# Performance work log

Hardware: AMD Instinct MI355X
Metric: run time of the kernel (lower is better)

Reference implementation:

```python
import jax, jax.numpy as jnp
from jax import lax
import numpy as np


def _conv3x3(x, w, b):
    # x: [B,C,H,W], w: [O,I,3,3] (OIHW), SAME padding, stride 1
    y = lax.conv_general_dilated(x, w, window_strides=(1, 1), padding='SAME',
                                 dimension_numbers=('NCHW', 'OIHW', 'NCHW'))
    return y + b[None, :, None, None]


def setup_inputs() -> dict:
    key = jax.random.key(0)
    ks = jax.random.split(key, 9)
    B, C, H, W = 4, 64, 64, 64
    wscale = 1.0 / np.sqrt(C * 9)  # keep conv outputs / attention logits sane
    x = jax.random.normal(ks[0], (B, C, H, W), dtype=jnp.float32)
    wq = jax.random.normal(ks[1], (C, C, 3, 3), dtype=jnp.float32) * wscale
    bq = jax.random.normal(ks[2], (C,), dtype=jnp.float32) * 0.1
    wk = jax.random.normal(ks[3], (C, C, 3, 3), dtype=jnp.float32) * wscale
    bk = jax.random.normal(ks[4], (C,), dtype=jnp.float32) * 0.1
    wv = jax.random.normal(ks[5], (C, C, 3, 3), dtype=jnp.float32) * wscale
    bv = jax.random.normal(ks[6], (C,), dtype=jnp.float32) * 0.1
    pos_gamma = jax.random.normal(ks[7], (1,), dtype=jnp.float32)
    chan_gamma = jax.random.normal(ks[8], (1,), dtype=jnp.float32)
    return {'x': x, 'wq': wq, 'bq': bq, 'wk': wk, 'bk': bk, 'wv': wv, 'bv': bv,
            'pos_gamma': pos_gamma, 'chan_gamma': chan_gamma}


def reference(x, wq, bq, wk, bk, wv, bv, pos_gamma, chan_gamma):
    B, C, H, W = x.shape
    N = H * W
    # position (spatial) self-attention over N = H*W locations
    q = _conv3x3(x, wq, bq).reshape(B, C, N)
    k = _conv3x3(x, wk, bk).reshape(B, C, N)
    v = _conv3x3(x, wv, bv).reshape(B, C, N)
    # attn[b,i,j] = softmax_j( sum_c q[b,c,i] * k[b,c,j] )
    pos_attn = jax.nn.softmax(jnp.einsum('bci,bcj->bij', q, k), axis=-1)
    # pos_out[b,c,j] = sum_i v[b,c,i] * attn[b,i,j]  (matches torch.bmm(v, attn))
    pos = jnp.einsum('bci,bij->bcj', v, pos_attn).reshape(B, C, H, W)
    pos_out = pos_gamma * pos + x
    # channel self-attention over C channels (x is its own q/k/v)
    xf = x.reshape(B, C, N)
    chan_attn = jax.nn.softmax(jnp.einsum('bcn,bdn->bcd', xf, xf), axis=-1)
    chan = jnp.einsum('bcd,bdn->bcn', chan_attn, xf).reshape(B, C, H, W)
    chan_out = chan_gamma * chan + x
    return pos_out + chan_out
```

## Files before the change

kernel.cpp:

```cpp
#include <hip/hip_runtime.h>

#define OFF_LP    0u
#define OFF_OP1   0u
#define OFF_XV2   65536u
#define OFF_GP    589824u
#define OFF_Q2    1048576u
#define OFF_K2    2097152u
#define OFF_V2    3145728u
#define OFF_X2    3670016u
#define OFF_WT    4194304u
#define OFF_A     4730880u
#define WS_FLOATS 4747264u

typedef short s8v __attribute__((ext_vector_type(8)));
typedef float f16v __attribute__((ext_vector_type(16)));

#define MFMA32(a, b, c) __builtin_amdgcn_mfma_f32_32x32x16_bf16((a), (b), (c), 0, 0, 0)

__device__ __forceinline__ unsigned short bf16_rne(float f) {
    union { float f; unsigned int u; } v; v.f = f;
    unsigned int r = v.u + 0x7FFFu + ((v.u >> 16) & 1u);
    return (unsigned short)(r >> 16);
}
__device__ __forceinline__ float bf2f(unsigned short h) {
    union { unsigned int u; float f; } t; t.u = ((unsigned int)h) << 16;
    return t.f;
}
__device__ __forceinline__ void split2(float f, unsigned short& h, unsigned short& l) {
    unsigned short hh = bf16_rne(f);
    h = hh;
    l = bf16_rne(f - bf2f(hh));
}
__device__ __forceinline__ unsigned int cvtpk(float lo, float hi) {
    unsigned int r;
    asm("v_cvt_pk_bf16_f32 %0, %1, %2" : "=v"(r) : "v"(lo), "v"(hi));
    return r;
}
__device__ __forceinline__ void pl32swap(unsigned int& a, unsigned int& b) {
    asm volatile("v_permlane32_swap_b32 %0, %1" : "+v"(a), "+v"(b));
}
__device__ __forceinline__ s8v mk8(unsigned int w0, unsigned int w1,
                                   unsigned int w2, unsigned int w3) {
    union { unsigned int u[4]; s8v v; } t;
    t.u[0] = w0; t.u[1] = w1; t.u[2] = w2; t.u[3] = w3;
    return t.v;
}
__device__ __forceinline__ f16v zero16() {
    f16v z;
#pragma unroll
    for (int i = 0; i < 16; ++i) z[i] = 0.0f;
    return z;
}


__global__ __launch_bounds__(256) void k_prep(
        const float* __restrict__ wq, const float* __restrict__ wk,
        const float* __restrict__ wv, const float* __restrict__ x,
        unsigned short* __restrict__ wf, unsigned short* __restrict__ X2,
        unsigned short* __restrict__ XV2) {
    int bid = blockIdx.x, tid = threadIdx.x;
    if (bid < 432) {
        int t = bid * 256 + tid;
        int f = t >> 9, pos = t & 511;
        int lane = pos >> 3, e = pos & 7;
        int oc = f & 1, kst = (f >> 1) & 3;
        int ct = f >> 3;
        int tap = ct % 9, conv = ct / 9;
        int o = oc * 32 + (lane & 31);
        int ci = kst * 16 + (lane >> 5) * 8 + e;
        const float* w = (conv == 0) ? wq : (conv == 1) ? wk : wv;
        float v = w[(o * 64 + ci) * 9 + tap];
        unsigned short hh, ll;
        split2(v, hh, ll);
        wf[(f * 2 + 0) * 512 + pos] = hh;
        wf[(f * 2 + 1) * 512 + pos] = ll;
    } else {
        int gid = (bid - 432) * 256 + tid;
        int b = gid >> 16;
        int c = (gid >> 10) & 63;
        int n4 = (gid & 1023) * 4;
        float4 v = *(const float4*)(x + (size_t)(b * 64 + c) * 4096 + n4);
        unsigned short hv[4] = {bf16_rne(v.x), bf16_rne(v.y), bf16_rne(v.z), bf16_rne(v.w)};
        int kst = c >> 4, e = c & 7, hb = (c >> 3) & 1;
#pragma unroll
        for (int u = 0; u < 4; ++u) {
            int n = n4 + u;
            int nch = n >> 5, lane = (n & 31) + 32 * hb;
            X2[(size_t)((b * 128 + nch) * 4 + kst) * 512 + lane * 8 + e] = hv[u];
        }
        int ich = n4 >> 5, ksub = (n4 >> 4) & 1, cb = c >> 5;
        int lane2 = (c & 31) + 32 * ((n4 >> 3) & 1);
        size_t xi = (size_t)(((b * 128 + ich) * 2 + ksub) * 2 + cb) * 512 + lane2 * 8 + (n4 & 7);
        unsigned long long w = (unsigned long long)hv[0]
                             | ((unsigned long long)hv[1] << 16)
                             | ((unsigned long long)hv[2] << 32)
                             | ((unsigned long long)hv[3] << 48);
        *(unsigned long long*)(XV2 + xi) = w;
    }
}

__global__ __launch_bounds__(384) void k_conv(
        const float* __restrict__ x, const unsigned short* __restrict__ wf,
        const float* __restrict__ bq, const float* __restrict__ bk, const float* __restrict__ bv,
        unsigned short* __restrict__ Q2, unsigned short* __restrict__ K2,
        unsigned short* __restrict__ V2) {
    int nb = blockIdx.x;
    int b = blockIdx.y;
    int h = nb >> 1, w0 = (nb & 1) * 32;

    __shared__ unsigned short xwh[6528];
    __shared__ unsigned short xwl[6528];

    int tid = threadIdx.x;
    for (int idx = tid; idx < 6528; idx += 384) {
        int W = idx % 34;
        int c = (idx / 34) & 63;
        int dy = idx / (34 * 64);
        int hs = h + dy - 1, wi = w0 + W - 1;
        float v = 0.0f;
        if (hs >= 0 && hs < 64 && wi >= 0 && wi < 64)
            v = x[((b * 64 + c) * 64 + hs) * 64 + wi];
        unsigned short hh_, ll_;
        split2(v, hh_, ll_);
        int row = dy * 34 + W;
        int byt = row * 128 + c * 2;
        int swz = byt ^ ((row & 7) << 4);
        *(unsigned short*)((char*)xwh + swz) = hh_;
        *(unsigned short*)((char*)xwl + swz) = ll_;
    }
    __syncthreads();

    int lane = tid & 63, wv = tid >> 6;
    int conv = wv >> 1, oc = wv & 1;
    int hh = lane >> 5, l31 = lane & 31;

    const float* bias = (conv == 0) ? bq : (conv == 1) ? bk : bv;
    f16v D;
    if (conv < 2) {
#pragma unroll
        for (int r = 0; r < 16; ++r)
            D[r] = bias[oc * 32 + (r & 3) + 8 * (r >> 2) + 4 * hh];
    } else {
        float bvv = bias[oc * 32 + l31];
#pragma unroll
        for (int r = 0; r < 16; ++r) D[r] = bvv;
    }

#pragma unroll
    for (int tap = 0; tap < 9; ++tap) {
        int dy = tap / 3, dx = tap % 3;
#pragma unroll
        for (int kst = 0; kst < 4; ++kst) {
            int f = ((conv * 9 + tap) * 4 + kst) * 2 + oc;
            s8v Wh = *(const s8v*)(wf + (f * 2 + 0) * 512 + lane * 8);
            s8v Wl = *(const s8v*)(wf + (f * 2 + 1) * 512 + lane * 8);
            int row = dy * 34 + dx + l31;
            int byt = row * 128 + kst * 32 + hh * 16;
            int swz = byt ^ ((row & 7) << 4);
            s8v Xh = *(const s8v*)((const char*)xwh + swz);
            s8v Xl = *(const s8v*)((const char*)xwl + swz);
            if (conv < 2) {
                D = MFMA32(Wh, Xh, D);
                D = MFMA32(Wh, Xl, D);
                D = MFMA32(Wl, Xh, D);
            } else {
                D = MFMA32(Xh, Wh, D);
                D = MFMA32(Xl, Wh, D);
                D = MFMA32(Xh, Wl, D);
            }
        }
    }

    if (conv < 2) {
        unsigned short sh[16], sl[16];
#pragma unroll
        for (int r = 0; r < 16; ++r) split2(D[r], sh[r], sl[r]);
        unsigned int ah0 = sh[0] | ((unsigned int)sh[1] << 16), ah1 = sh[2] | ((unsigned int)sh[3] << 16);
        unsigned int ah2 = sh[4] | ((unsigned int)sh[5] << 16), ah3 = sh[6] | ((unsigned int)sh[7] << 16);
        pl32swap(ah0, ah2); pl32swap(ah1, ah3);
        s8v F0h = mk8(ah0, ah1, ah2, ah3);
        unsigned int al0 = sl[0] | ((unsigned int)sl[1] << 16), al1 = sl[2] | ((unsigned int)sl[3] << 16);
        unsigned int al2 = sl[4] | ((unsigned int)sl[5] << 16), al3 = sl[6] | ((unsigned int)sl[7] << 16);
        pl32swap(al0, al2); pl32swap(al1, al3);
        s8v F0l = mk8(al0, al1, al2, al3);
        unsigned int bh0 = sh[8] | ((unsigned int)sh[9] << 16), bh1 = sh[10] | ((unsigned int)sh[11] << 16);
        unsigned int bh2 = sh[12] | ((unsigned int)sh[13] << 16), bh3 = sh[14] | ((unsigned int)sh[15] << 16);
        pl32swap(bh0, bh2); pl32swap(bh1, bh3);
        s8v F1h = mk8(bh0, bh1, bh2, bh3);
        unsigned int bl0 = sl[8] | ((unsigned int)sl[9] << 16), bl1 = sl[10] | ((unsigned int)sl[11] << 16);
        unsigned int bl2 = sl[12] | ((unsigned int)sl[13] << 16), bl3 = sl[14] | ((unsigned int)sl[15] << 16);
        pl32swap(bl0, bl2); pl32swap(bl1, bl3);
        s8v F1l = mk8(bl0, bl1, bl2, bl3);
        unsigned short* dst = (conv == 0) ? Q2 : K2;
        size_t b0 = (size_t)(((b * 128 + nb) * 4 + oc * 2 + 0) * 2) * 512 + lane * 8;
        size_t b1 = (size_t)(((b * 128 + nb) * 4 + oc * 2 + 1) * 2) * 512 + lane * 8;
        *(s8v*)(dst + b0) = F0h;
        *(s8v*)(dst + b0 + 512) = F0l;
        *(s8v*)(dst + b1) = F1h;
        *(s8v*)(dst + b1 + 512) = F1l;
    } else {
        unsigned int a0 = cvtpk(D[0], D[1]),  a1 = cvtpk(D[2], D[3]);
        unsigned int a2 = cvtpk(D[4], D[5]),  a3 = cvtpk(D[6], D[7]);
        pl32swap(a0, a2); pl32swap(a1, a3);
        s8v F0h = mk8(a0, a1, a2, a3);
        unsigned int b0w = cvtpk(D[8], D[9]),  b1w = cvtpk(D[10], D[11]);
        unsigned int b2w = cvtpk(D[12], D[13]), b3w = cvtpk(D[14], D[15]);
        pl32swap(b0w, b2w); pl32swap(b1w, b3w);
        s8v F1h = mk8(b0w, b1w, b2w, b3w);
        size_t v0 = (size_t)(((b * 128 + nb) * 2 + 0) * 2 + oc) * 512 + lane * 8;
        size_t v1 = (size_t)(((b * 128 + nb) * 2 + 1) * 2 + oc) * 512 + lane * 8;
        *(s8v*)(V2 + v0) = F0h;
        *(s8v*)(V2 + v1) = F1h;
    }
}

__global__ __launch_bounds__(256) void k_gram(const unsigned short* __restrict__ XV2,
                                              float* __restrict__ Gp) {
    int kp = blockIdx.x, b = blockIdx.y;
    int tid = threadIdx.x, lane = tid & 63, wv = tid >> 6;
    int cb1 = wv & 1, cb2 = wv >> 1;
    f16v G = zero16();
#pragma unroll
    for (int t = 0; t < 8; ++t) {
        int ich = kp * 8 + t;
        const unsigned short* base = XV2 + (size_t)(b * 128 + ich) * 2048 + lane * 8;
        s8v a0 = *(const s8v*)(base + (0 * 2 + cb1) * 512);
        s8v b0 = *(const s8v*)(base + (0 * 2 + cb2) * 512);
        s8v a1 = *(const s8v*)(base + (1 * 2 + cb1) * 512);
        s8v b1 = *(const s8v*)(base + (1 * 2 + cb2) * 512);
        G = MFMA32(a0, b0, G);
        G = MFMA32(a1, b1, G);
    }
    int hh = lane >> 5, l31 = lane & 31;
#pragma unroll
    for (int r = 0; r < 16; ++r) {
        int cc = cb1 * 32 + (r & 3) + 8 * (r >> 2) + 4 * hh;
        int dd = cb2 * 32 + l31;
        Gp[(size_t)(kp * 4 + b) * 4096 + cc * 64 + dd] = G[r];
    }
}

__global__ void k_asm(const float* __restrict__ Gp, unsigned short* __restrict__ A2) {
    int row = blockIdx.x;
    int d = threadIdx.x;
    int b = row >> 6, c = row & 63;
    float g = 0.0f;
#pragma unroll
    for (int p = 0; p < 16; ++p) g += Gp[(size_t)(p * 4 + b) * 4096 + c * 64 + d];
    float mx = g;
    for (int off = 32; off >= 1; off >>= 1) mx = fmaxf(mx, __shfl_xor(mx, off, 64));
    float e = __expf(g - mx);
    float s = e;
    for (int off = 32; off >= 1; off >>= 1) s += __shfl_xor(s, off, 64);
    float a = e / s;
    int cb = c >> 5, kst = d >> 4;
    int lane2 = (c & 31) + 32 * ((d >> 3) & 1);
    A2[(size_t)((b * 2 + cb) * 4 + kst) * 512 + lane2 * 8 + (d & 7)] = bf16_rne(a);
}

__global__ __launch_bounds__(512, 2) void k_pass1(
        const unsigned short* __restrict__ Q2, const unsigned short* __restrict__ K2,
        float* __restrict__ lpart) {
    int flat = blockIdx.x;
    int xcd = flat & 7;
    int b = xcd >> 1;
    int rest = (xcd & 1) * 64 + (flat >> 3);
    int ichp = rest & 63, jh = rest >> 6;
    int ich0 = ichp * 2;
    int tid = threadIdx.x, lane = tid & 63, wv = tid >> 6;

    __shared__ float lsum[8][2][32];

    const unsigned short* qp = Q2 + (size_t)(b * 128 + ich0) * 4096 + lane * 8;
    s8v q0f0 = *(const s8v*)(qp);
    s8v q0f1 = *(const s8v*)(qp + 512);
    s8v q0f2 = *(const s8v*)(qp + 1024);
    s8v q0f3 = *(const s8v*)(qp + 1536);
    s8v q0f4 = *(const s8v*)(qp + 2048);
    s8v q0f5 = *(const s8v*)(qp + 2560);
    s8v q0f6 = *(const s8v*)(qp + 3072);
    s8v q0f7 = *(const s8v*)(qp + 3584);
    s8v q1f0 = *(const s8v*)(qp + 4096);
    s8v q1f1 = *(const s8v*)(qp + 4608);
    s8v q1f2 = *(const s8v*)(qp + 5120);
    s8v q1f3 = *(const s8v*)(qp + 5632);
    s8v q1f4 = *(const s8v*)(qp + 6144);
    s8v q1f5 = *(const s8v*)(qp + 6656);
    s8v q1f6 = *(const s8v*)(qp + 7168);
    s8v q1f7 = *(const s8v*)(qp + 7680);

    float la0 = 0.f, la1 = 0.f, lb0 = 0.f, lb1 = 0.f;
#pragma unroll 1
    for (int t = 0; t < 8; ++t) {
        int jch = jh * 64 + wv * 8 + t;
        const unsigned short* kp = K2 + (size_t)(b * 128 + jch) * 4096 + lane * 8;
        s8v kf0 = *(const s8v*)(kp);
        s8v kf1 = *(const s8v*)(kp + 512);
        s8v kf2 = *(const s8v*)(kp + 1024);
        s8v kf3 = *(const s8v*)(kp + 1536);
        s8v kf4 = *(const s8v*)(kp + 2048);
        s8v kf5 = *(const s8v*)(kp + 2560);
        s8v kf6 = *(const s8v*)(kp + 3072);
        s8v kf7 = *(const s8v*)(kp + 3584);
        {
            f16v Sa = zero16(), Sb = zero16();
            Sa = MFMA32(kf0, q0f0, Sa);
            Sa = MFMA32(kf0, q0f1, Sa);
            Sa = MFMA32(kf1, q0f0, Sa);
            Sa = MFMA32(kf2, q0f2, Sa);
            Sa = MFMA32(kf2, q0f3, Sa);
            Sa = MFMA32(kf3, q0f2, Sa);
            Sb = MFMA32(kf4, q0f4, Sb);
            Sb = MFMA32(kf4, q0f5, Sb);
            Sb = MFMA32(kf5, q0f4, Sb);
            Sb = MFMA32(kf6, q0f6, Sb);
            Sb = MFMA32(kf6, q0f7, Sb);
            Sb = MFMA32(kf7, q0f6, Sb);
#pragma unroll
            for (int r = 0; r < 8; ++r) la0 += __expf(Sa[r] + Sb[r]);
#pragma unroll
            for (int r = 8; r < 16; ++r) la1 += __expf(Sa[r] + Sb[r]);
        }
        {
            f16v Sa = zero16(), Sb = zero16();
            Sa = MFMA32(kf0, q1f0, Sa);
            Sa = MFMA32(kf0, q1f1, Sa);
            Sa = MFMA32(kf1, q1f0, Sa);
            Sa = MFMA32(kf2, q1f2, Sa);
            Sa = MFMA32(kf2, q1f3, Sa);
            Sa = MFMA32(kf3, q1f2, Sa);
            Sb = MFMA32(kf4, q1f4, Sb);
            Sb = MFMA32(kf4, q1f5, Sb);
            Sb = MFMA32(kf5, q1f4, Sb);
            Sb = MFMA32(kf6, q1f6, Sb);
            Sb = MFMA32(kf6, q1f7, Sb);
            Sb = MFMA32(kf7, q1f6, Sb);
#pragma unroll
            for (int r = 0; r < 8; ++r) lb0 += __expf(Sa[r] + Sb[r]);
#pragma unroll
            for (int r = 8; r < 16; ++r) lb1 += __expf(Sa[r] + Sb[r]);
        }
    }
    float lacc0 = la0 + la1;
    lacc0 += __shfl_xor(lacc0, 32);
    float lacc1 = lb0 + lb1;
    lacc1 += __shfl_xor(lacc1, 32);
    if (lane < 32) {
        lsum[wv][0][lane] = lacc0;
        lsum[wv][1][lane] = lacc1;
    }
    __syncthreads();
    if (tid < 64) {
        int ic = tid >> 5, iL = tid & 31;
        float s = 0.f;
#pragma unroll
        for (int p = 0; p < 8; ++p) s += lsum[p][ic][iL];
        lpart[jh * 16384 + b * 4096 + (ich0 + ic) * 32 + iL] = s;
    }
}

__global__ __launch_bounds__(256) void k_mvn(
        unsigned short* __restrict__ V2, const float* __restrict__ lpart) {
    int u = blockIdx.x * 256 + threadIdx.x;
    int lane = u & 63, ksub = (u >> 7) & 1;
    int ich = (u >> 8) & 127, b = u >> 15;
    int n0 = ich * 32 + ksub * 16 + (lane >> 5) * 8;
    size_t base = (size_t)u * 8;
    s8v vh = *(s8v*)(V2 + base);
    const float* l0 = lpart + b * 4096 + n0;
    float4 a0 = *(const float4*)(l0);
    float4 a1 = *(const float4*)(l0 + 4);
    float4 c0 = *(const float4*)(l0 + 16384);
    float4 c1 = *(const float4*)(l0 + 16384 + 4);
    float lv[8] = {a0.x + c0.x, a0.y + c0.y, a0.z + c0.z, a0.w + c0.w,
                   a1.x + c1.x, a1.y + c1.y, a1.z + c1.z, a1.w + c1.w};
    s8v o;
#pragma unroll
    for (int e = 0; e < 8; ++e) {
        float inv = 1.0f / lv[e];
        o[e] = (short)bf16_rne(bf2f((unsigned short)vh[e]) * inv);
    }
    *(s8v*)(V2 + base) = o;
}

__global__ __launch_bounds__(512, 2) void k_pass2(
        const unsigned short* __restrict__ Q2, const unsigned short* __restrict__ K2,
        const unsigned short* __restrict__ V2, float* __restrict__ outp,
        float* __restrict__ op1) {
    int flat = blockIdx.x;
    int xcd = flat & 7;
    int b = xcd >> 1;
    int rest = (xcd & 1) * 64 + (flat >> 3);
    int jtp = rest & 63, ih = rest >> 6;
    int jt0 = jtp * 2;
    int tid = threadIdx.x, lane = tid & 63, wv = tid >> 6;

    __shared__ float smem[12288];
    unsigned short* Klds = (unsigned short*)(smem + 8192);
    float* rl = smem;

    {
        const unsigned short* ksrc = K2 + (size_t)(b * 128 + jt0) * 4096;
#pragma unroll
        for (int s = 0; s < 2; ++s) {
            int seg = tid + s * 512;
            *(s8v*)(Klds + seg * 8) = *(const s8v*)(ksrc + seg * 8);
        }
    }
    __syncthreads();

    f16v O0a = zero16(), O1a = zero16();
    f16v O0b = zero16(), O1b = zero16();

#pragma unroll 1
    for (int t = 0; t < 8; ++t) {
        int ich = ih * 64 + wv * 8 + t;
        const unsigned short* qp = Q2 + (size_t)(b * 128 + ich) * 4096 + lane * 8;
        s8v qf0 = *(const s8v*)(qp);
        s8v qf1 = *(const s8v*)(qp + 512);
        s8v qf2 = *(const s8v*)(qp + 1024);
        s8v qf3 = *(const s8v*)(qp + 1536);
        s8v qf4 = *(const s8v*)(qp + 2048);
        s8v qf5 = *(const s8v*)(qp + 2560);
        s8v qf6 = *(const s8v*)(qp + 3072);
        s8v qf7 = *(const s8v*)(qp + 3584);
        const unsigned short* vp = V2 + (size_t)(b * 128 + ich) * 2048 + lane * 8;
        s8v vA = *(const s8v*)(vp);
        s8v vB = *(const s8v*)(vp + 512);
        s8v vC = *(const s8v*)(vp + 1024);
        s8v vD = *(const s8v*)(vp + 1536);

#pragma unroll
        for (int js = 0; js < 2; ++js) {
            const unsigned short* kl = Klds + js * 4096 + lane * 8;
            s8v kf0 = *(const s8v*)(kl);
            s8v kf1 = *(const s8v*)(kl + 512);
            s8v kf2 = *(const s8v*)(kl + 1024);
            s8v kf3 = *(const s8v*)(kl + 1536);
            s8v kf4 = *(const s8v*)(kl + 2048);
            s8v kf5 = *(const s8v*)(kl + 2560);
            s8v kf6 = *(const s8v*)(kl + 3072);
            s8v kf7 = *(const s8v*)(kl + 3584);

            f16v Sa = zero16(), Sb = zero16();
            Sa = MFMA32(qf0, kf0, Sa);
            Sa = MFMA32(qf0, kf1, Sa);
            Sa = MFMA32(qf1, kf0, Sa);
            Sa = MFMA32(qf2, kf2, Sa);
            Sa = MFMA32(qf2, kf3, Sa);
            Sa = MFMA32(qf3, kf2, Sa);
            Sb = MFMA32(qf4, kf4, Sb);
            Sb = MFMA32(qf4, kf5, Sb);
            Sb = MFMA32(qf5, kf4, Sb);
            Sb = MFMA32(qf6, kf6, Sb);
            Sb = MFMA32(qf6, kf7, Sb);
            Sb = MFMA32(qf7, kf6, Sb);

            float p[16];
#pragma unroll
            for (int r = 0; r < 16; ++r) p[r] = __expf(Sa[r] + Sb[r]);

            unsigned int a0 = cvtpk(p[0], p[1]),  a1 = cvtpk(p[2], p[3]);
            unsigned int a2 = cvtpk(p[4], p[5]),  a3 = cvtpk(p[6], p[7]);
            pl32swap(a0, a2);
            pl32swap(a1, a3);
            s8v P0 = mk8(a0, a1, a2, a3);
            unsigned int b0 = cvtpk(p[8], p[9]),  b1 = cvtpk(p[10], p[11]);
            unsigned int b2 = cvtpk(p[12], p[13]), b3 = cvtpk(p[14], p[15]);
            pl32swap(b0, b2);
            pl32swap(b1, b3);
            s8v P1 = mk8(b0, b1, b2, b3);

            if (js == 0) {
                O0a = MFMA32(vA, P0, O0a);
                O0a = MFMA32(vC, P1, O0a);
                O1a = MFMA32(vB, P0, O1a);
                O1a = MFMA32(vD, P1, O1a);
            } else {
                O0b = MFMA32(vA, P0, O0b);
                O0b = MFMA32(vC, P1, O0b);
                O1b = MFMA32(vB, P0, O1b);
                O1b = MFMA32(vD, P1, O1b);
            }
        }
    }

    int hh = lane >> 5, jj = lane & 31;
    float s0[4], s1[4];
    if (wv < 4) {
#pragma unroll
        for (int r = 0; r < 16; ++r) {
            int c = (r & 3) + 8 * (r >> 2) + 4 * hh;
            rl[(wv * 64 + c) * 32 + jj] = O0a[r];
            rl[(wv * 64 + c + 32) * 32 + jj] = O1a[r];
        }
    }
    __syncthreads();
#pragma unroll
    for (int k = 0; k < 4; ++k) {
        int el = tid + k * 512;
        s0[k] = ((rl[el] + rl[2048 + el]) + rl[4096 + el]) + rl[6144 + el];
    }
    __syncthreads();
    if (wv >= 4) {
#pragma unroll
        for (int r = 0; r < 16; ++r) {
            int c = (r & 3) + 8 * (r >> 2) + 4 * hh;
            rl[((wv - 4) * 64 + c) * 32 + jj] = O0a[r];
            rl[((wv - 4) * 64 + c + 32) * 32 + jj] = O1a[r];
        }
    }
    __syncthreads();
#pragma unroll
    for (int k = 0; k < 4; ++k) {
        int el = tid + k * 512;
        s0[k] = ((s0[k] + rl[el]) + rl[2048 + el]) + rl[4096 + el];
        s0[k] += rl[6144 + el];
    }
    __syncthreads();
    if (wv < 4) {
#pragma unroll
        for (int r = 0; r < 16; ++r) {
            int c = (r & 3) + 8 * (r >> 2) + 4 * hh;
            rl[(wv * 64 + c) * 32 + jj] = O0b[r];
            rl[(wv * 64 + c + 32) * 32 + jj] = O1b[r];
        }
    }
    __syncthreads();
#pragma unroll
    for (int k = 0; k < 4; ++k) {
        int el = tid + k * 512;
        s1[k] = ((rl[el] + rl[2048 + el]) + rl[4096 + el]) + rl[6144 + el];
    }
    __syncthreads();
    if (wv >= 4) {
#pragma unroll
        for (int r = 0; r < 16; ++r) {
            int c = (r & 3) + 8 * (r >> 2) + 4 * hh;
            rl[((wv - 4) * 64 + c) * 32 + jj] = O0b[r];
            rl[((wv - 4) * 64 + c + 32) * 32 + jj] = O1b[r];
        }
    }
    __syncthreads();
#pragma unroll
    for (int k = 0; k < 4; ++k) {
        int el = tid + k * 512;
        s1[k] = ((s1[k] + rl[el]) + rl[2048 + el]) + rl[4096 + el];
        s1[k] += rl[6144 + el];
    }

    float* dst = ih ? op1 : outp;
#pragma unroll
    for (int k = 0; k < 4; ++k) {
        int el = tid + k * 512;
        int c = el >> 5, j2 = el & 31;
        size_t ob = (size_t)(b * 64 + c) * 4096 + jtp * 64;
        dst[ob + j2] = s0[k];
        dst[ob + 32 + j2] = s1[k];
    }
}

__global__ __launch_bounds__(256) void k_final(
        const float* __restrict__ op1, const unsigned short* __restrict__ X2,
        const unsigned short* __restrict__ A2, const float* __restrict__ x,
        const float* __restrict__ pg, const float* __restrict__ cg,
        float* __restrict__ out) {
    int flat = blockIdx.x;
    int xcd = flat & 7;
    int b = xcd >> 1;
    int jtp = (xcd & 1) * 32 + (flat >> 3);
    int jt0 = jtp * 2;
    int tid = threadIdx.x, lane = tid & 63, wv = tid >> 6;
    int hh = lane >> 5, jj = lane & 31;

    __shared__ float chan[64 * 65];

    {
        int jts = wv >> 1, cb = wv & 1;
        f16v Dc = zero16();
#pragma unroll
        for (int kst = 0; kst < 4; ++kst) {
            s8v af = *(const s8v*)(A2 + (size_t)((b * 2 + cb) * 4 + kst) * 512 + lane * 8);
            s8v xf = *(const s8v*)(X2 + (size_t)((b * 128 + jt0 + jts) * 4 + kst) * 512 + lane * 8);
            Dc = MFMA32(af, xf, Dc);
        }
#pragma unroll
        for (int r = 0; r < 16; ++r) {
            int c = cb * 32 + (r & 3) + 8 * (r >> 2) + 4 * hh;
            chan[c * 65 + jts * 32 + jj] = Dc[r];
        }
    }
    __syncthreads();
    float pgv = pg[0], cgv = cg[0];
#pragma unroll
    for (int k = 0; k < 16; ++k) {
        int el = tid + k * 256;
        int c = el >> 6, j2 = el & 63;
        size_t loc = (size_t)(b * 64 + c) * 4096 + jtp * 64 + j2;
        float pos = out[loc] + op1[loc];
        out[loc] = pgv * pos + cgv * chan[c * 65 + j2] + 2.0f * x[loc];
    }
}

extern "C" void kernel_launch(void* const* d_in, const int* in_sizes, int n_in,
                              void* d_out, int out_size, void* d_ws, size_t ws_size,
                              hipStream_t stream) {
    const float* x  = (const float*)d_in[0];
    const float* wq = (const float*)d_in[1];
    const float* bq = (const float*)d_in[2];
    const float* wk = (const float*)d_in[3];
    const float* bk = (const float*)d_in[4];
    const float* wv = (const float*)d_in[5];
    const float* bv = (const float*)d_in[6];
    const float* pg = (const float*)d_in[7];
    const float* cg = (const float*)d_in[8];
    float* out = (float*)d_out;

    if (ws_size < (size_t)WS_FLOATS * sizeof(float)) return;
    float* ws = (float*)d_ws;
    float* lpart = ws + OFF_LP;
    float* op1   = ws + OFF_OP1;
    unsigned short* XV2 = (unsigned short*)(ws + OFF_XV2);
    float* Gp = ws + OFF_GP;
    unsigned short* Q2  = (unsigned short*)(ws + OFF_Q2);
    unsigned short* K2  = (unsigned short*)(ws + OFF_K2);
    unsigned short* V2  = (unsigned short*)(ws + OFF_V2);
    unsigned short* X2  = (unsigned short*)(ws + OFF_X2);
    unsigned short* wfb = (unsigned short*)(ws + OFF_WT);
    unsigned short* A2  = (unsigned short*)(ws + OFF_A);

    k_prep<<<1456, 256, 0, stream>>>(wq, wk, wv, x, wfb, X2, XV2);
    k_conv<<<dim3(128, 4), 384, 0, stream>>>(x, wfb, bq, bk, bv, Q2, K2, V2);
    k_gram<<<dim3(16, 4), 256, 0, stream>>>(XV2, Gp);
    k_asm<<<256, 64, 0, stream>>>(Gp, A2);
    k_pass1<<<512, 512, 0, stream>>>(Q2, K2, lpart);
    k_mvn<<<512, 256, 0, stream>>>(V2, lpart);
    k_pass2<<<512, 512, 0, stream>>>(Q2, K2, V2, out, op1);
    k_final<<<256, 256, 0, stream>>>(op1, X2, A2, x, pg, cg, out);
}
```

Measured before the change: 115.8 us.

## Fuse final epilogue into pass2 and drop the split over query halves

```diff
diff --git a/kernel.cpp b/kernel.cpp
--- a/kernel.cpp
+++ b/kernel.cpp
@@ -1,7 +1,6 @@
 #include <hip/hip_runtime.h>
 
 #define OFF_LP    0u
-#define OFF_OP1   0u
 #define OFF_XV2   65536u
 #define OFF_GP    589824u
 #define OFF_Q2    1048576u
@@ -383,15 +382,16 @@
     *(s8v*)(V2 + base) = o;
 }
 
-__global__ __launch_bounds__(512, 2) void k_pass2(
+__global__ __launch_bounds__(512) void k_pass2(
         const unsigned short* __restrict__ Q2, const unsigned short* __restrict__ K2,
-        const unsigned short* __restrict__ V2, float* __restrict__ outp,
-        float* __restrict__ op1) {
+        const unsigned short* __restrict__ V2, const unsigned short* __restrict__ X2,
+        const unsigned short* __restrict__ A2, const float* __restrict__ x,
+        const float* __restrict__ pg, const float* __restrict__ cg,
+        float* __restrict__ out) {
     int flat = blockIdx.x;
     int xcd = flat & 7;
     int b = xcd >> 1;
-    int rest = (xcd & 1) * 64 + (flat >> 3);
-    int jtp = rest & 63, ih = rest >> 6;
+    int jtp = (xcd & 1) * 32 + (flat >> 3);
     int jt0 = jtp * 2;
     int tid = threadIdx.x, lane = tid & 63, wv = tid >> 6;
 
@@ -412,9 +412,9 @@
     f16v O0a = zero16(), O1a = zero16();
     f16v O0b = zero16(), O1b = zero16();
 
-#pragma unroll 1
-    for (int t = 0; t < 8; ++t) {
-        int ich = ih * 64 + wv * 8 + t;
+#pragma unroll 2
+    for (int t = 0; t < 16; ++t) {
+        int ich = wv * 16 + t;
         const unsigned short* qp = Q2 + (size_t)(b * 128 + ich) * 4096 + lane * 8;
         s8v qf0 = *(const s8v*)(qp);
         s8v qf1 = *(const s8v*)(qp + 512);
@@ -548,57 +548,40 @@
         s1[k] = ((s1[k] + rl[el]) + rl[2048 + el]) + rl[4096 + el];
         s1[k] += rl[6144 + el];
     }
-
-    float* dst = ih ? op1 : outp;
+    __syncthreads();
+
+    float* chan = smem;
+    float* xres = smem + 4160;
+    if (wv < 4) {
+        int jts = wv >> 1, cb = wv & 1;
+        f16v Dc = zero16();
+#pragma unroll
+        for (int kst = 0; kst < 4; ++kst) {
+            s8v af = *(const s8v*)(A2 + (size_t)((b * 2 + cb) * 4 + kst) * 512 + lane * 8);
+            s8v xf = *(const s8v*)(X2 + (size_t)((b * 128 + jt0 + jts) * 4 + kst) * 512 + lane * 8);
+            Dc = MFMA32(af, xf, Dc);
+        }
+#pragma unroll
+        for (int r = 0; r < 16; ++r) {
+            int c = cb * 32 + (r & 3) + 8 * (r >> 2) + 4 * hh;
+            chan[c * 65 + jts * 32 + jj] = Dc[r];
+        }
+    }
+#pragma unroll
+    for (int k = 0; k < 8; ++k) {
+        int el = tid + k * 512;
+        int c = el >> 6, j2 = el & 63;
+        xres[el] = x[(size_t)(b * 64 + c) * 4096 + jtp * 64 + j2];
+    }
+    __syncthreads();
+    float pgv = pg[0], cgv = cg[0];
 #pragma unroll
     for (int k = 0; k < 4; ++k) {
         int el = tid + k * 512;
         int c = el >> 5, j2 = el & 31;
         size_t ob = (size_t)(b * 64 + c) * 4096 + jtp * 64;
-        dst[ob + j2] = s0[k];
-        dst[ob + 32 + j2] = s1[k];
-    }
-}
-
-__global__ __launch_bounds__(256) void k_final(
-        const float* __restrict__ op1, const unsigned short* __restrict__ X2,
-        const unsigned short* __restrict__ A2, const float* __restrict__ x,
-        const float* __restrict__ pg, const float* __restrict__ cg,
-        float* __restrict__ out) {
-    int flat = blockIdx.x;
-    int xcd = flat & 7;
-    int b = xcd >> 1;
-    int jtp = (xcd & 1) * 32 + (flat >> 3);
-    int jt0 = jtp * 2;
-    int tid = threadIdx.x, lane = tid & 63, wv = tid >> 6;
-    int hh = lane >> 5, jj = lane & 31;
-
-    __shared__ float chan[64 * 65];
-
-    {
-        int jts = wv >> 1, cb = wv & 1;
-        f16v Dc = zero16();
-#pragma unroll
-        for (int kst = 0; kst < 4; ++kst) {
-            s8v af = *(const s8v*)(A2 + (size_t)((b * 2 + cb) * 4 + kst) * 512 + lane * 8);
-            s8v xf = *(const s8v*)(X2 + (size_t)((b * 128 + jt0 + jts) * 4 + kst) * 512 + lane * 8);
-            Dc = MFMA32(af, xf, Dc);
-        }
-#pragma unroll
-        for (int r = 0; r < 16; ++r) {
-            int c = cb * 32 + (r & 3) + 8 * (r >> 2) + 4 * hh;
-            chan[c * 65 + jts * 32 + jj] = Dc[r];
-        }
-    }
-    __syncthreads();
-    float pgv = pg[0], cgv = cg[0];
-#pragma unroll
-    for (int k = 0; k < 16; ++k) {
-        int el = tid + k * 256;
-        int c = el >> 6, j2 = el & 63;
-        size_t loc = (size_t)(b * 64 + c) * 4096 + jtp * 64 + j2;
-        float pos = out[loc] + op1[loc];
-        out[loc] = pgv * pos + cgv * chan[c * 65 + j2] + 2.0f * x[loc];
+        out[ob + j2] = pgv * s0[k] + cgv * chan[c * 65 + j2] + 2.0f * xres[c * 64 + j2];
+        out[ob + 32 + j2] = pgv * s1[k] + cgv * chan[c * 65 + 32 + j2] + 2.0f * xres[c * 64 + 32 + j2];
     }
 }
 
@@ -619,7 +602,6 @@
     if (ws_size < (size_t)WS_FLOATS * sizeof(float)) return;
     float* ws = (float*)d_ws;
     float* lpart = ws + OFF_LP;
-    float* op1   = ws + OFF_OP1;
     unsigned short* XV2 = (unsigned short*)(ws + OFF_XV2);
     float* Gp = ws + OFF_GP;
     unsigned short* Q2  = (unsigned short*)(ws + OFF_Q2);
@@ -635,6 +617,5 @@
     k_asm<<<256, 64, 0, stream>>>(Gp, A2);
     k_pass1<<<512, 512, 0, stream>>>(Q2, K2, lpart);
     k_mvn<<<512, 256, 0, stream>>>(V2, lpart);
-    k_pass2<<<512, 512, 0, stream>>>(Q2, K2, V2, out, op1);
-    k_final<<<256, 256, 0, stream>>>(op1, X2, A2, x, pg, cg, out);
-}
+    k_pass2<<<256, 512, 0, stream>>>(Q2, K2, V2, X2, A2, x, pg, cg, out);
+}
```

After: 106.3 us. 1.09x faster.
